# Kernel tuning notes

Hardware: AMD Instinct MI355X
Metric: run time of the kernel (lower is better)

The kernel has to match this reference:

```python
import jax, jax.numpy as jnp
import numpy as np

N_NODES = 50000
N_EDGES = 800000
DIM_IN = 128
DIM_H = 128
DIM_OUT = 8
N_GRAPHS = 32


def _glorot(key, shape):
    fan_in, fan_out = shape[0], shape[1]
    lim = float(np.sqrt(6.0 / (fan_in + fan_out)))
    return jax.random.uniform(key, shape, jnp.float32, -lim, lim)


def setup_inputs() -> dict:
    key = jax.random.key(0)
    ks = jax.random.split(key, 16)
    x = jax.random.normal(ks[0], (N_NODES, DIM_IN), jnp.float32)
    edge_index = jax.random.randint(ks[1], (2, N_EDGES), 0, N_NODES, jnp.int64)
    batch = jnp.sort(jax.random.randint(ks[2], (N_NODES,), 0, N_GRAPHS, jnp.int64))
    inp = {"x": x, "edge_index": edge_index, "batch": batch}
    # SAGEConv layers: lin_l (aggregated neighbors, with bias) + lin_r (self, no bias)
    dims = [(DIM_IN, DIM_H), (DIM_H, DIM_H), (DIM_H, DIM_H)]
    for i, (di, do) in enumerate(dims, start=1):
        inp[f"Wl{i}"] = _glorot(ks[2 + 3 * i], (di, do))
        inp[f"bl{i}"] = jnp.zeros((do,), jnp.float32)
        inp[f"Wr{i}"] = _glorot(ks[3 + 3 * i], (di, do))
    inp["W_lin1"] = _glorot(ks[13], (DIM_H, DIM_H))
    inp["b_lin1"] = jnp.zeros((DIM_H,), jnp.float32)
    inp["W_lin2"] = _glorot(ks[14], (DIM_H, DIM_OUT))
    inp["b_lin2"] = jnp.zeros((DIM_OUT,), jnp.float32)
    return inp


def _sage_conv(x, src, dst, Wl, bl, Wr):
    # mean aggregation of source-node features at destination nodes
    agg = jax.ops.segment_sum(x[src], dst, num_segments=N_NODES)
    cnt = jax.ops.segment_sum(jnp.ones((src.shape[0], 1), x.dtype), dst, num_segments=N_NODES)
    agg = agg / jnp.maximum(cnt, 1.0)
    return agg @ Wl + bl + x @ Wr


def reference(x, edge_index, batch, Wl1, bl1, Wr1, Wl2, bl2, Wr2, Wl3, bl3, Wr3,
              W_lin1, b_lin1, W_lin2, b_lin2):
    src, dst = edge_index[0], edge_index[1]
    h = jax.nn.relu(_sage_conv(x, src, dst, Wl1, bl1, Wr1))
    h = jax.nn.relu(_sage_conv(h, src, dst, Wl2, bl2, Wr2))
    h = jax.nn.relu(_sage_conv(h, src, dst, Wl3, bl3, Wr3))
    # global mean pool over graphs in the batch
    pooled = jax.ops.segment_sum(h, batch, num_segments=N_GRAPHS)
    gcnt = jax.ops.segment_sum(jnp.ones((h.shape[0], 1), h.dtype), batch, num_segments=N_GRAPHS)
    pooled = pooled / jnp.maximum(gcnt, 1.0)
    h = jax.nn.relu(pooled @ W_lin1 + b_lin1)
    # dropout p=0.5 is identity in eval mode
    return h @ W_lin2 + b_lin2
```

## Files before the change

### kernel.cpp

```cpp
#include <hip/hip_runtime.h>
#include <hip/hip_bf16.h>

#define N_NODES 50000
#define N_EDGES 800000
#define DIM 128
#define N_GRAPHS 32
#define CAP 64
#define NPS 128
#define NSUP 391
#define SBCAP2 2432
#define EPB 8192
#define EPT 32
#define NBLK ((N_EDGES + EPB - 1) / EPB)
#define AGG_NPB 16

#define CVT_BLKS (N_NODES * DIM / 4 / 256)
#define RPK_BLKS ((6 * 16384 + 255) / 256)
#define ZRO_BLKS ((N_GRAPHS * DIM + 255) / 256)
#define PREP_BLKS (CVT_BLKS + RPK_BLKS + ZRO_BLKS)

typedef _Float16 f16;
typedef __attribute__((ext_vector_type(2))) _Float16 f16x2;
typedef __attribute__((ext_vector_type(4))) _Float16 f16x4;
typedef __attribute__((ext_vector_type(8))) _Float16 f16x8;
typedef __attribute__((ext_vector_type(4))) float f32x4;

__global__ __launch_bounds__(256) void k_prep(const float* __restrict__ x,
                                              f16* __restrict__ h16,
                                              const float* __restrict__ W0, const float* __restrict__ W1,
                                              const float* __restrict__ W2, const float* __restrict__ W3,
                                              const float* __restrict__ W4, const float* __restrict__ W5,
                                              f16* __restrict__ pack,
                                              float* __restrict__ pooled,
                                              int* __restrict__ gcnt,
                                              int* __restrict__ gCnt) {
  int blk = blockIdx.x;
  if (blk < CVT_BLKS) {
    int idx = blk * 256 + threadIdx.x;
    f32x4 v = *(const f32x4*)(x + idx * 4);
    f16x4 h;
    #pragma unroll
    for (int j = 0; j < 4; ++j) h[j] = (f16)v[j];
    *(f16x4*)(h16 + idx * 4) = h;
    return;
  }
  blk -= CVT_BLKS;
  if (blk < RPK_BLKS) {
    int idx = blk * 256 + threadIdx.x;
    if (idx >= 6 * 16384) return;
    int m = idx >> 14, r = idx & 16383;
    const float* W = m == 0 ? W0 : m == 1 ? W1 : m == 2 ? W2 : m == 3 ? W3 : m == 4 ? W4 : W5;
    int ct = r >> 11, ks = (r >> 9) & 3, l = (r >> 3) & 63, j = r & 7;
    int k = ks * 32 + ((l >> 4) << 3) + j;
    int c = ct * 16 + (l & 15);
    pack[m * 16384 + r] = (f16)W[k * DIM + c];
    return;
  }
  blk -= RPK_BLKS;
  int i = blk * 256 + threadIdx.x;
  if (i < N_GRAPHS * DIM) pooled[i] = 0.f;
  if (i < N_GRAPHS) gcnt[i] = 0;
  if (i < NSUP) gCnt[i] = 0;
}

__global__ __launch_bounds__(256) void k_part2(const int* __restrict__ src,
                                               const int* __restrict__ dst,
                                               int* __restrict__ gCnt,
                                               unsigned int* __restrict__ sbBuf) {
  __shared__ int hist[NSUP];
  __shared__ int base[NSUP];
  int tid = threadIdx.x;
  int e0 = blockIdx.x * EPB;
  int nE = min(EPB, N_EDGES - e0);
  for (int i = tid; i < NSUP; i += 256) hist[i] = 0;
  __syncthreads();
  unsigned pk[EPT];
  #pragma unroll
  for (int j = 0; j < EPT; ++j) {
    int idx = j * 256 + tid;
    if (idx < nE) {
      int e = e0 + idx;
      int d = dst[e], s = src[e];
      int sb = d >> 7;
      pk[j] = ((unsigned)sb << 23) | ((unsigned)(d & 127) << 16) | (unsigned)s;
      atomicAdd(&hist[sb], 1);
    } else pk[j] = 0xFFFFFFFFu;
  }
  __syncthreads();
  for (int i = tid; i < NSUP; i += 256) {
    int h = hist[i];
    base[i] = h ? atomicAdd(&gCnt[i], h) : 0;
    hist[i] = 0;
  }
  __syncthreads();
  #pragma unroll
  for (int j = 0; j < EPT; ++j) {
    unsigned p = pk[j];
    if (p != 0xFFFFFFFFu) {
      int sb = p >> 23;
      int slot = base[sb] + atomicAdd(&hist[sb], 1);
      if (slot < SBCAP2)
        sbBuf[(size_t)sb * SBCAP2 + slot] = p & 0x7FFFFFu;
    }
  }
}

__global__ __launch_bounds__(256) void k_bin(const int* __restrict__ gCnt,
                                             const unsigned int* __restrict__ sbBuf,
                                             int* __restrict__ cnt,
                                             unsigned short* __restrict__ esrc) {
  __shared__ unsigned short buck[NPS * CAP];
  __shared__ int cl[NPS];
  int sb = blockIdx.x, tid = threadIdx.x;
  for (int i = tid; i < NPS; i += 256) cl[i] = 0;
  __syncthreads();
  int n = min(gCnt[sb], SBCAP2);
  const unsigned int* buf = sbBuf + (size_t)sb * SBCAP2;
  for (int i = tid; i < n; i += 256) {
    unsigned p = buf[i];
    int dl = p >> 16;
    int slot = atomicAdd(&cl[dl], 1);
    if (slot < CAP) buck[dl * CAP + slot] = (unsigned short)(p & 0xFFFF);
  }
  __syncthreads();
  size_t basep = (size_t)sb * NPS * CAP;
  for (int i = tid; i < NPS * CAP; i += 256)
    esrc[basep + i] = buck[i];
  int n0 = sb * NPS;
  for (int d = tid; d < NPS; d += 256) {
    int node = n0 + d;
    if (node < N_NODES) cnt[node] = min(cl[d], CAP);
  }
}

__global__ __launch_bounds__(256) void k_agg(const f16* __restrict__ H16,
                                             const int* __restrict__ cnt,
                                             const unsigned short* __restrict__ esrc,
                                             f16* __restrict__ agg16) {
  int wid = threadIdx.x >> 6;
  int lane = threadIdx.x & 63;
  int l16 = lane & 15;
  int sg = lane >> 4;
  int node0 = blockIdx.x * AGG_NPB + wid * 4;

  #pragma unroll
  for (int nl = 0; nl < 4; ++nl) {
    int node = node0 + nl;
    int dcnt = cnt[node];
    int b = node * CAP, e = b + dcnt;

    f32x4 aA0 = (f32x4){0.f,0.f,0.f,0.f}, aA1 = aA0, aB0 = aA0, aB1 = aA0,
          aC0 = aA0, aC1 = aA0, aD0 = aA0, aD1 = aA0;
    int i = b + sg;
    for (; i + 12 < e; i += 16) {
      int s0 = esrc[i], s1 = esrc[i + 4], s2 = esrc[i + 8], s3 = esrc[i + 12];
      f16x8 v0 = *(const f16x8*)(H16 + (size_t)s0 * DIM + l16 * 8);
      f16x8 v1 = *(const f16x8*)(H16 + (size_t)s1 * DIM + l16 * 8);
      f16x8 v2 = *(const f16x8*)(H16 + (size_t)s2 * DIM + l16 * 8);
      f16x8 v3 = *(const f16x8*)(H16 + (size_t)s3 * DIM + l16 * 8);
      #pragma unroll
      for (int j = 0; j < 4; ++j) {
        aA0[j] += (float)v0[j]; aA1[j] += (float)v0[4 + j];
        aB0[j] += (float)v1[j]; aB1[j] += (float)v1[4 + j];
        aC0[j] += (float)v2[j]; aC1[j] += (float)v2[4 + j];
        aD0[j] += (float)v3[j]; aD1[j] += (float)v3[4 + j];
      }
    }
    for (; i < e; i += 4) {
      int s = esrc[i];
      f16x8 v = *(const f16x8*)(H16 + (size_t)s * DIM + l16 * 8);
      #pragma unroll
      for (int j = 0; j < 4; ++j) { aA0[j] += (float)v[j]; aA1[j] += (float)v[4 + j]; }
    }
    #pragma unroll
    for (int j = 0; j < 4; ++j) {
      aA0[j] = (aA0[j] + aB0[j]) + (aC0[j] + aD0[j]);
      aA1[j] = (aA1[j] + aB1[j]) + (aC1[j] + aD1[j]);
    }
    #pragma unroll
    for (int j = 0; j < 4; ++j) {
      aA0[j] += __shfl_xor(aA0[j], 16, 64);
      aA1[j] += __shfl_xor(aA1[j], 16, 64);
      aA0[j] += __shfl_xor(aA0[j], 32, 64);
      aA1[j] += __shfl_xor(aA1[j], 32, 64);
    }
    if (lane < 16) {
      float inv = 1.0f / (float)max(dcnt, 1);
      f16x8 r;
      #pragma unroll
      for (int j = 0; j < 4; ++j) {
        r[j] = (f16)(aA0[j] * inv);
        r[4 + j] = (f16)(aA1[j] * inv);
      }
      *(f16x8*)(agg16 + (size_t)node * DIM + l16 * 8) = r;
    }
  }
}

template<bool POOL>
__global__ __launch_bounds__(256) void k_gemm(const f16* __restrict__ Agg16,
                                              const f16* __restrict__ Hprev16,
                                              const f16* __restrict__ packWl,
                                              const f16* __restrict__ packWr,
                                              const float* __restrict__ bias,
                                              f16* __restrict__ Hout16,
                                              const int* __restrict__ batch,
                                              float* __restrict__ pooled,
                                              int* __restrict__ gcnt) {
  __shared__ f16 wlds[16384];
  __shared__ float lpoolw[4][2][DIM];
  __shared__ int bshared[64];
  int tid = threadIdx.x;
  int wid = tid >> 6, l = tid & 63;
  int row0blk = blockIdx.x * 64;
  int row0 = row0blk + wid * 16;
  int arow = row0 + (l & 15);
  int arowc = min(arow, N_NODES - 1);
  int koff = (l >> 4) << 3;

  if (POOL) {
    if (tid < 64) {
      int r = row0blk + tid;
      bshared[tid] = (r < N_NODES) ? batch[r] : -1;
    }
  }

  f32x4 acc[8];
  #pragma unroll
  for (int ct = 0; ct < 8; ++ct) acc[ct] = (f32x4){0.f, 0.f, 0.f, 0.f};

  #pragma unroll
  for (int mat = 0; mat < 2; ++mat) {
    const f16* A = (mat ? Hprev16 : Agg16) + (size_t)arowc * DIM + koff;
    f16x8 aa[4];
    #pragma unroll
    for (int ks = 0; ks < 4; ++ks) aa[ks] = *(const f16x8*)(A + ks * 32);

    const f16* P = mat ? packWr : packWl;
    if (mat) __syncthreads();
    #pragma unroll
    for (int it = 0; it < 8; ++it) {
      int idx = (it * 256 + tid) * 8;
      *(f16x8*)&wlds[idx] = *(const f16x8*)&P[idx];
    }
    __syncthreads();

    #pragma unroll
    for (int ct = 0; ct < 8; ++ct) {
      #pragma unroll
      for (int ks = 0; ks < 4; ++ks) {
        f16x8 bfrag = *(const f16x8*)&wlds[((ct * 4 + ks) * 64 + l) * 8];
        acc[ct] = __builtin_amdgcn_mfma_f32_16x16x32_f16(aa[ks], bfrag, acc[ct], 0, 0, 0);
      }
    }
  }

  int drowb = row0 + ((l >> 4) << 2);
  int c0 = l & 15;
  int g0 = POOL ? bshared[0] : 0;
  #pragma unroll
  for (int ct = 0; ct < 8; ++ct) {
    int c = ct * 16 + c0;
    float bb = bias[c];
    float ps0 = 0.f, ps1 = 0.f;
    #pragma unroll
    for (int i = 0; i < 4; ++i) {
      int r = drowb + i;
      if (r < N_NODES) {
        float v = acc[ct][i] + bb;
        v = v > 0.f ? v : 0.f;
        if (POOL) {
          if (bshared[r - row0blk] == g0) ps0 += v; else ps1 += v;
        } else {
          Hout16[(size_t)r * DIM + c] = (f16)v;
        }
      }
    }
    if (POOL) {
      ps0 += __shfl_xor(ps0, 16, 64); ps0 += __shfl_xor(ps0, 32, 64);
      ps1 += __shfl_xor(ps1, 16, 64); ps1 += __shfl_xor(ps1, 32, 64);
      if (l < 16) {
        lpoolw[wid][0][c] = ps0;
        lpoolw[wid][1][c] = ps1;
      }
    }
  }

  if (POOL) {
    __syncthreads();
    int rlast = min(row0blk + 63, N_NODES - 1);
    int g1 = bshared[rlast - row0blk];
    int slot = tid >> 7, c = tid & 127;
    float s = lpoolw[0][slot][c] + lpoolw[1][slot][c] +
              lpoolw[2][slot][c] + lpoolw[3][slot][c];
    int g = slot ? g1 : g0;
    atomicAdd(&pooled[g * DIM + c], s);
    if (tid == 0) {
      int c0n = 0, c1n = 0;
      #pragma unroll 8
      for (int i = 0; i < 64; ++i) {
        int b = bshared[i];
        if (b == g0) c0n++;
        else if (b >= 0) c1n++;
      }
      atomicAdd(&gcnt[g0], c0n);
      if (c1n) atomicAdd(&gcnt[g1], c1n);
    }
  }
}

__global__ __launch_bounds__(128) void k_mlp(const float* __restrict__ pooled,
                                             const int* __restrict__ gcnt,
                                             const float* __restrict__ W1,
                                             const float* __restrict__ b1,
                                             const float* __restrict__ W2,
                                             const float* __restrict__ b2,
                                             float* __restrict__ out) {
  int g = blockIdx.x, c = threadIdx.x;
  __shared__ float pn[DIM];
  __shared__ float h1[DIM];
  pn[c] = pooled[g * DIM + c] / (float)max(gcnt[g], 1);
  __syncthreads();
  float s = b1[c];
  #pragma unroll 8
  for (int k = 0; k < DIM; ++k) s += pn[k] * W1[k * DIM + c];
  h1[c] = s > 0.f ? s : 0.f;
  __syncthreads();
  if (c < 8) {
    float s2 = b2[c];
    #pragma unroll 8
    for (int k = 0; k < DIM; ++k) s2 += h1[k] * W2[k * 8 + c];
    out[g * 8 + c] = s2;
  }
}

extern "C" void kernel_launch(void* const* d_in, const int* in_sizes, int n_in,
                              void* d_out, int out_size, void* d_ws, size_t ws_size,
                              hipStream_t stream) {
  const float* x = (const float*)d_in[0];
  const int* ei = (const int*)d_in[1];
  const int* src = ei;
  const int* dst = ei + N_EDGES;
  const int* batch = (const int*)d_in[2];
  const float* Wl1 = (const float*)d_in[3];  const float* bl1 = (const float*)d_in[4];  const float* Wr1 = (const float*)d_in[5];
  const float* Wl2 = (const float*)d_in[6];  const float* bl2 = (const float*)d_in[7];  const float* Wr2 = (const float*)d_in[8];
  const float* Wl3 = (const float*)d_in[9];  const float* bl3 = (const float*)d_in[10]; const float* Wr3 = (const float*)d_in[11];
  const float* W_1 = (const float*)d_in[12]; const float* b_1 = (const float*)d_in[13];
  const float* W_2 = (const float*)d_in[14]; const float* b_2 = (const float*)d_in[15];

  char* ws = (char*)d_ws;
  size_t off = 0;
  auto alloc = [&](size_t bytes) {
    void* p = ws + off;
    off += (bytes + 255) & ~(size_t)255;
    return p;
  };
  f16* agg16 = (f16*)alloc((size_t)N_NODES * DIM * 2);
  f16* h16A  = (f16*)alloc((size_t)N_NODES * DIM * 2);
  f16* h16B  = (f16*)alloc((size_t)N_NODES * DIM * 2);
  int* cnt   = (int*)alloc(N_NODES * 4);
  unsigned short* esrc = (unsigned short*)alloc((size_t)NSUP * NPS * CAP * 2);
  unsigned int* sbBuf  = (unsigned int*)alloc((size_t)NSUP * SBCAP2 * 4);
  f16* pack  = (f16*)alloc(6 * 16384 * sizeof(f16));
  float* pooled = (float*)alloc(N_GRAPHS * DIM * 4);
  int* gcnt = (int*)alloc(N_GRAPHS * 4);
  int* gCnt = (int*)alloc(NSUP * 4);

  k_prep<<<PREP_BLKS, 256, 0, stream>>>(x, h16A, Wl1, Wr1, Wl2, Wr2, Wl3, Wr3,
                                        pack, pooled, gcnt, gCnt);
  k_part2<<<NBLK, 256, 0, stream>>>(src, dst, gCnt, sbBuf);
  k_bin<<<NSUP, 256, 0, stream>>>(gCnt, sbBuf, cnt, esrc);

  const int gemmBlocks = (N_NODES + 63) / 64;
  const int aggBlocks = N_NODES / AGG_NPB;
  k_agg<<<aggBlocks, 256, 0, stream>>>(h16A, cnt, esrc, agg16);
  k_gemm<false><<<gemmBlocks, 256, 0, stream>>>(agg16, h16A, pack + 0 * 16384, pack + 1 * 16384, bl1, h16B, nullptr, nullptr, nullptr);
  k_agg<<<aggBlocks, 256, 0, stream>>>(h16B, cnt, esrc, agg16);
  k_gemm<false><<<gemmBlocks, 256, 0, stream>>>(agg16, h16B, pack + 2 * 16384, pack + 3 * 16384, bl2, h16A, nullptr, nullptr, nullptr);
  k_agg<<<aggBlocks, 256, 0, stream>>>(h16A, cnt, esrc, agg16);
  k_gemm<true><<<gemmBlocks, 256, 0, stream>>>(agg16, h16A, pack + 4 * 16384, pack + 5 * 16384, bl3, nullptr, batch, pooled, gcnt);

  k_mlp<<<N_GRAPHS, 128, 0, stream>>>(pooled, gcnt, W_1, b_1, W_2, b_2, (float*)d_out);
}
```

Baseline: 205.2 us.

## Split aggregation across feature slices so each wave gathers 16 edges concurrently

The gather-aggregate kernel now launches four blocks per node group, each handling a 32-feature slice of the 128-wide row. Within a wave, 4 lanes cover the slice and 16 row slots walk edges in parallel, replacing the prior 16-lane-by-4-edge layout with manual 4-way unroll. This raises edge-level parallelism per node (average degree is about 16) and cuts loop trip counts. In exchange each gather is only 64 bytes per row, esrc and cnt are re-read by four blocks, and the shuffle reduction now takes four steps instead of two.

```diff
diff --git a/kernel.cpp b/kernel.cpp
--- a/kernel.cpp
+++ b/kernel.cpp
@@ -13,6 +13,7 @@
 #define EPT 32
 #define NBLK ((N_EDGES + EPB - 1) / EPB)
 #define AGG_NPB 16
+#define NSLICE 4
 
 #define CVT_BLKS (N_NODES * DIM / 4 / 256)
 #define RPK_BLKS ((6 * 16384 + 255) / 256)
@@ -137,11 +138,14 @@
                                              const int* __restrict__ cnt,
                                              const unsigned short* __restrict__ esrc,
                                              f16* __restrict__ agg16) {
+  int slice = blockIdx.x & (NSLICE - 1);
+  int group = blockIdx.x >> 2;
   int wid = threadIdx.x >> 6;
   int lane = threadIdx.x & 63;
-  int l16 = lane & 15;
-  int sg = lane >> 4;
-  int node0 = blockIdx.x * AGG_NPB + wid * 4;
+  int rowslot = lane >> 2;
+  int l4 = lane & 3;
+  int dimoff = slice * 32 + l4 * 8;
+  int node0 = group * AGG_NPB + wid * 4;
 
   #pragma unroll
   for (int nl = 0; nl < 4; ++nl) {
@@ -149,50 +153,29 @@
     int dcnt = cnt[node];
     int b = node * CAP, e = b + dcnt;
 
-    f32x4 aA0 = (f32x4){0.f,0.f,0.f,0.f}, aA1 = aA0, aB0 = aA0, aB1 = aA0,
-          aC0 = aA0, aC1 = aA0, aD0 = aA0, aD1 = aA0;
-    int i = b + sg;
-    for (; i + 12 < e; i += 16) {
-      int s0 = esrc[i], s1 = esrc[i + 4], s2 = esrc[i + 8], s3 = esrc[i + 12];
-      f16x8 v0 = *(const f16x8*)(H16 + (size_t)s0 * DIM + l16 * 8);
-      f16x8 v1 = *(const f16x8*)(H16 + (size_t)s1 * DIM + l16 * 8);
-      f16x8 v2 = *(const f16x8*)(H16 + (size_t)s2 * DIM + l16 * 8);
-      f16x8 v3 = *(const f16x8*)(H16 + (size_t)s3 * DIM + l16 * 8);
+    f32x4 a0 = (f32x4){0.f, 0.f, 0.f, 0.f}, a1 = a0;
+    for (int i = b + rowslot; i < e; i += 16) {
+      int s = esrc[i];
+      f16x8 v = *(const f16x8*)(H16 + (size_t)s * DIM + dimoff);
       #pragma unroll
-      for (int j = 0; j < 4; ++j) {
-        aA0[j] += (float)v0[j]; aA1[j] += (float)v0[4 + j];
-        aB0[j] += (float)v1[j]; aB1[j] += (float)v1[4 + j];
-        aC0[j] += (float)v2[j]; aC1[j] += (float)v2[4 + j];
-        aD0[j] += (float)v3[j]; aD1[j] += (float)v3[4 + j];
-      }
-    }
-    for (; i < e; i += 4) {
-      int s = esrc[i];
-      f16x8 v = *(const f16x8*)(H16 + (size_t)s * DIM + l16 * 8);
-      #pragma unroll
-      for (int j = 0; j < 4; ++j) { aA0[j] += (float)v[j]; aA1[j] += (float)v[4 + j]; }
+      for (int j = 0; j < 4; ++j) { a0[j] += (float)v[j]; a1[j] += (float)v[4 + j]; }
     }
     #pragma unroll
     for (int j = 0; j < 4; ++j) {
-      aA0[j] = (aA0[j] + aB0[j]) + (aC0[j] + aD0[j]);
-      aA1[j] = (aA1[j] + aB1[j]) + (aC1[j] + aD1[j]);
-    }
-    #pragma unroll
-    for (int j = 0; j < 4; ++j) {
-      aA0[j] += __shfl_xor(aA0[j], 16, 64);
-      aA1[j] += __shfl_xor(aA1[j], 16, 64);
-      aA0[j] += __shfl_xor(aA0[j], 32, 64);
-      aA1[j] += __shfl_xor(aA1[j], 32, 64);
-    }
-    if (lane < 16) {
+      a0[j] += __shfl_xor(a0[j], 4, 64);  a1[j] += __shfl_xor(a1[j], 4, 64);
+      a0[j] += __shfl_xor(a0[j], 8, 64);  a1[j] += __shfl_xor(a1[j], 8, 64);
+      a0[j] += __shfl_xor(a0[j], 16, 64); a1[j] += __shfl_xor(a1[j], 16, 64);
+      a0[j] += __shfl_xor(a0[j], 32, 64); a1[j] += __shfl_xor(a1[j], 32, 64);
+    }
+    if (rowslot == 0) {
       float inv = 1.0f / (float)max(dcnt, 1);
       f16x8 r;
       #pragma unroll
       for (int j = 0; j < 4; ++j) {
-        r[j] = (f16)(aA0[j] * inv);
-        r[4 + j] = (f16)(aA1[j] * inv);
-      }
-      *(f16x8*)(agg16 + (size_t)node * DIM + l16 * 8) = r;
+        r[j] = (f16)(a0[j] * inv);
+        r[4 + j] = (f16)(a1[j] * inv);
+      }
+      *(f16x8*)(agg16 + (size_t)node * DIM + dimoff) = r;
     }
   }
 }
@@ -372,7 +355,7 @@
   k_bin<<<NSUP, 256, 0, stream>>>(gCnt, sbBuf, cnt, esrc);
 
   const int gemmBlocks = (N_NODES + 63) / 64;
-  const int aggBlocks = N_NODES / AGG_NPB;
+  const int aggBlocks = (N_NODES / AGG_NPB) * NSLICE;
   k_agg<<<aggBlocks, 256, 0, stream>>>(h16A, cnt, esrc, agg16);
   k_gemm<false><<<gemmBlocks, 256, 0, stream>>>(agg16, h16A, pack + 0 * 16384, pack + 1 * 16384, bl1, h16B, nullptr, nullptr, nullptr);
   k_agg<<<aggBlocks, 256, 0, stream>>>(h16B, cnt, esrc, agg16);
```

New measurement: 302.4 us. 47.4% more time.
